# Optimization experiments

Measured on AMD Instinct MI355X. Metric: run time of the kernel, lower is better.

The kernel has to match this reference:

```python
import jax, jax.numpy as jnp
import numpy as np

# Model constants (match init_kwargs)
H, P, N, G, NL, K = 32, 64, 128, 1, 15, 4   # heads, head_dim, state, groups, lambda levels, conv width
HID, T, BATCH = 1024, 1024, 1
INTER = H * P                    # 2048
CONV_DIM = INTER + 2 * G * N     # 2304
PROJ = INTER + CONV_DIM + H * (NL + 1)  # 4864
EPS = 1e-5


def _level_matrix(t_len: int) -> np.ndarray:
    """Fenwick-tree level assignment: for query t, prefix [0,t] splits into
    power-of-two segments from binary expansion of t+1; segment of length 2^l -> level l."""
    lm = np.zeros((t_len, t_len), dtype=np.int32)
    for t in range(t_len):
        n = t + 1
        while n > 0:
            lb = n & (-n)
            lm[t, n - lb:n] = lb.bit_length() - 1
            n -= lb
    return lm


def setup_inputs() -> dict:
    key = jax.random.key(0)
    ks = jax.random.split(key, 4)
    return {
        "hidden_states": jax.random.normal(ks[0], (BATCH, T, HID), jnp.float32),
        "in_proj_w": jax.random.normal(ks[1], (PROJ, HID), jnp.float32) / np.sqrt(HID).astype(np.float32),
        "in_proj_b": jnp.zeros((PROJ,), jnp.float32),
        "conv_w": jax.random.normal(ks[2], (CONV_DIM, K), jnp.float32) / np.sqrt(K).astype(np.float32),
        "dt_bias": jnp.ones((H,), jnp.float32),
        "A_log": jnp.log(jnp.arange(1, H + 1, dtype=jnp.float32)),
        "L_param": jnp.ones((H, NL), jnp.float32),
        "D": jnp.ones((H,), jnp.float32),
        "rmsnorm_w": jnp.ones((INTER,), jnp.float32),
        "out_proj_w": jax.random.normal(ks[3], (HID, INTER), jnp.float32) / np.sqrt(INTER).astype(np.float32),
        "out_proj_b": jnp.zeros((HID,), jnp.float32),
        "level_mat": jnp.asarray(_level_matrix(T)),  # (T,T) int32, data-independent
    }


def reference(hidden_states, in_proj_w, in_proj_b, conv_w, dt_bias, A_log,
              L_param, D, rmsnorm_w, out_proj_w, out_proj_b, level_mat):
    b, t, _ = hidden_states.shape
    # in_proj and split: [z | xBC | dt | dl]
    zxbcdtdl = hidden_states @ in_proj_w.T + in_proj_b
    z, xBC, dt, dl = jnp.split(zxbcdtdl, [INTER, INTER + CONV_DIM, INTER + CONV_DIM + H], axis=-1)
    # depthwise causal conv1d (width K) + SiLU
    xp = jnp.pad(xBC, ((0, 0), (K - 1, 0), (0, 0)))
    conv = sum(xp[:, w:w + t, :] * conv_w[:, w] for w in range(K))
    xBC = jax.nn.silu(conv)
    x, Bm, Cm = jnp.split(xBC, [INTER, INTER + G * N], axis=-1)
    x = x.reshape(b, t, H, P)          # v pre-scale
    Bm = Bm.reshape(b, t, G, N)        # keys
    Cm = Cm.reshape(b, t, G, N)        # queries
    dl = dl.reshape(b, t, H, NL)
    # D residual uses unscaled x (matches hmamba_chunk_scan_combined ordering)
    D_res = x * D[None, None, :, None]
    dt = jax.nn.softplus(dt + dt_bias)            # (b,t,H)
    v = x * dt[..., None]                          # (b,t,H,P)
    A = -jnp.exp(A_log)                            # (H,)
    g = A * dt                                     # (b,t,H), per-token log-decay (<=0)
    Ls = jax.nn.softplus(L_param * dl)             # (b,t,H,NL) per-token level scales
    # cumulative log-decay; decay(t,s) = exp(cg_t - cg_s), s<=t
    cg = jnp.cumsum(g, axis=1).transpose(0, 2, 1)  # (b,H,t)
    mask = jnp.tril(jnp.ones((t, t), bool))
    logdecay = jnp.where(mask, cg[:, :, :, None] - cg[:, :, None, :], -jnp.inf)
    decay = jnp.exp(logdecay)                      # (b,H,t,s)
    # hierarchical level scale H[t,s] = Ls[b,t,h, level(t,s)]
    Hmat = jnp.take_along_axis(Ls.transpose(0, 2, 1, 3), level_mat[None, None, :, :], axis=-1)  # (b,H,t,s)
    scores = jnp.einsum('btgn,bsgn->bgts', Cm, Bm)  # (b,G,t,s), G=1 broadcasts over heads
    att = scores * decay * Hmat                     # (b,H,t,s), masked via decay=0
    y = jnp.einsum('bhts,bshp->bthp', att, v) + D_res
    y = y.reshape(b, t, INTER)
    # gated RMSNorm with norm_before_gate=False: normalize(y * silu(z)) * w
    yg = y * jax.nn.silu(z)
    y = yg * jax.lax.rsqrt(jnp.mean(yg * yg, axis=-1, keepdims=True) + EPS) * rmsnorm_w
    return y @ out_proj_w.T + out_proj_b
```

## Files before the change

kernel.cpp:

```cpp
#include <hip/hip_runtime.h>
#include <hip/hip_bf16.h>
#include <math.h>

#define T_LEN 1024
#define HID 1024
#define NHEAD 32
#define HDIM 64
#define NSTATE 128
#define NLVL 15
#define KCONV 4
#define INTER 2048
#define CONV_DIM 2304
#define PROJ 4864
#define EPS 1e-5f
#define TPROJ ((size_t)T_LEN * PROJ)

typedef __attribute__((ext_vector_type(8))) _Float16 half8;
typedef __attribute__((ext_vector_type(4))) _Float16 half4;
typedef __attribute__((ext_vector_type(4))) float float4v;
typedef unsigned short ushort_t;

__device__ __forceinline__ float softplus_f(float x) {
  return fmaxf(x, 0.f) + log1pf(expf(-fabsf(x)));
}
__device__ __forceinline__ float silu_f(float x) {
  return x / (1.f + expf(-x));
}
__device__ __forceinline__ ushort_t f2h(float f) {
  union { _Float16 h; ushort_t u; } v;
  v.h = (_Float16)f;
  return v.u;
}
__device__ __forceinline__ float h2f(ushort_t u) {
  union { ushort_t u; _Float16 h; } v;
  v.u = u;
  return (float)v.h;
}
__device__ __forceinline__ void gload_lds16(const void* g, void* l) {
  __builtin_amdgcn_global_load_lds(
      (const __attribute__((address_space(1))) void*)g,
      (__attribute__((address_space(3))) void*)l, 16, 0, 0);
}

#define N4_HS  (T_LEN * HID / 4)
#define N4_WI  (PROJ * HID / 4)
#define N4_WO  (HID * INTER / 4)
__global__ __launch_bounds__(256) void prep_f16(
    const float* __restrict__ hs, const float* __restrict__ wi,
    const float* __restrict__ wo, ushort_t* __restrict__ hsb,
    ushort_t* __restrict__ wib, ushort_t* __restrict__ wob) {
  int i = blockIdx.x * 256 + threadIdx.x;
  const float* src; ushort_t* dst; int j;
  if (i < N4_HS)              { src = hs; dst = hsb; j = i; }
  else if (i < N4_HS + N4_WI) { src = wi; dst = wib; j = i - N4_HS; }
  else                        { src = wo; dst = wob; j = i - N4_HS - N4_WI; }
  float4 v = reinterpret_cast<const float4*>(src)[j];
  union { ushort_t u[4]; unsigned long long ll; } o;
  o.u[0] = f2h(v.x); o.u[1] = f2h(v.y); o.u[2] = f2h(v.z); o.u[3] = f2h(v.w);
  reinterpret_cast<unsigned long long*>(dst)[j] = o.ll;
}

__global__ __launch_bounds__(256) void gemm_f16_sk(
    const ushort_t* __restrict__ A, const ushort_t* __restrict__ B,
    ushort_t* __restrict__ Cpart, int M, int N, int K, int Kc) {
  __shared__ ushort_t As[2][128][32];
  __shared__ ushort_t Bs[2][128][32];
  const int tid = threadIdx.x;
  const int w = tid >> 6, L = tid & 63;
  const int n0 = blockIdx.x * 128, m0 = blockIdx.y * 128;
  const int kbeg = blockIdx.z * Kc;
  ushort_t* __restrict__ C = Cpart + (size_t)blockIdx.z * M * N;
  const int mq = (w & 1) * 64, nq = (w >> 1) * 64;
  const int srow = (L >> 2);
  const int sch = (L & 3) * 8;

  float4v acc[4][4];
#pragma unroll
  for (int i = 0; i < 4; ++i)
#pragma unroll
    for (int j = 0; j < 4; ++j) acc[i][j] = (float4v){0.f, 0.f, 0.f, 0.f};

  const int niter = Kc / 32;
  {
    const int kk = kbeg;
#pragma unroll
    for (int j = 0; j < 2; ++j) {
      int r0 = 16 * (w * 2 + j);
      gload_lds16(A + (size_t)(m0 + r0 + srow) * K + kk + sch, &As[0][r0][0]);
      gload_lds16(B + (size_t)(n0 + r0 + srow) * K + kk + sch, &Bs[0][r0][0]);
    }
  }
  for (int it = 0; it < niter; ++it) {
    __syncthreads();
    if (it + 1 < niter) {
      const int kk = kbeg + (it + 1) * 32;
      const int nb = (it + 1) & 1;
#pragma unroll
      for (int j = 0; j < 2; ++j) {
        int r0 = 16 * (w * 2 + j);
        gload_lds16(A + (size_t)(m0 + r0 + srow) * K + kk + sch, &As[nb][r0][0]);
        gload_lds16(B + (size_t)(n0 + r0 + srow) * K + kk + sch, &Bs[nb][r0][0]);
      }
    }
    const int cb = it & 1;
    half8 af[4], bf[4];
#pragma unroll
    for (int t = 0; t < 4; ++t) {
      af[t] = *reinterpret_cast<const half8*>(&As[cb][mq + t * 16 + (L & 15)][(L >> 4) * 8]);
      bf[t] = *reinterpret_cast<const half8*>(&Bs[cb][nq + t * 16 + (L & 15)][(L >> 4) * 8]);
    }
#pragma unroll
    for (int mt = 0; mt < 4; ++mt)
#pragma unroll
      for (int nt = 0; nt < 4; ++nt)
        acc[mt][nt] = __builtin_amdgcn_mfma_f32_16x16x32_f16(af[mt], bf[nt], acc[mt][nt], 0, 0, 0);
  }
  const int qrow = (L >> 4) * 4;
#pragma unroll
  for (int mt = 0; mt < 4; ++mt) {
#pragma unroll
    for (int nt = 0; nt < 4; ++nt) {
      int col = n0 + nq + nt * 16 + (L & 15);
#pragma unroll
      for (int r = 0; r < 4; ++r) {
        int row = m0 + mq + mt * 16 + qrow + r;
        C[(size_t)row * N + col] = f2h(acc[mt][nt][r]);
      }
    }
  }
}

__global__ __launch_bounds__(256) void reduce_out8(const ushort_t* __restrict__ p,
                                                   const float* __restrict__ bias,
                                                   float* __restrict__ out, int MN) {
  int i = blockIdx.x * 256 + threadIdx.x;
  if (i * 8 >= MN) return;
  float o[8] = {0.f, 0.f, 0.f, 0.f, 0.f, 0.f, 0.f, 0.f};
#pragma unroll
  for (int z = 0; z < 8; ++z) {
    half8 v = reinterpret_cast<const half8*>(p + (size_t)z * MN)[i];
#pragma unroll
    for (int j = 0; j < 8; ++j) o[j] += (float)v[j];
  }
  int col = (i * 8) & (HID - 1);
#pragma unroll
  for (int j = 0; j < 8; ++j) o[j] += bias[col + j];
  float4 o0 = {o[0], o[1], o[2], o[3]}, o1 = {o[4], o[5], o[6], o[7]};
  reinterpret_cast<float4*>(out)[i * 2] = o0;
  reinterpret_cast<float4*>(out)[i * 2 + 1] = o1;
}

__global__ __launch_bounds__(64) void scan_g(
    const ushort_t* __restrict__ zh, const float* __restrict__ in_b,
    const float* __restrict__ dt_bias, const float* __restrict__ A_log,
    float* __restrict__ dtb, double* __restrict__ cgd) {
  const int h = blockIdx.x, l = threadIdx.x;
  const int c = INTER + CONV_DIM + h;
  const float bb = in_b[c] + dt_bias[h];
  const float Ae = -expf(A_log[h]);
  double pre[16];
  double acc = 0.0;
#pragma unroll
  for (int i = 0; i < 16; ++i) {
    int t = l * 16 + i;
    size_t o = (size_t)t * PROJ + c;
    float x = h2f(zh[o]) + h2f(zh[TPROJ + o]) + h2f(zh[2 * TPROJ + o]) +
              h2f(zh[3 * TPROJ + o]) + bb;
    float dt = softplus_f(x);
    dtb[t * NHEAD + h] = dt;
    acc += (double)(Ae * dt);
    pre[i] = acc;
  }
  double s = acc;
#pragma unroll
  for (int off = 1; off < 64; off <<= 1) {
    double o = __shfl_up(s, off, 64);
    if (l >= off) s += o;
  }
  const double base = s - acc;
  double* cr = cgd + (size_t)h * T_LEN + l * 16;
#pragma unroll
  for (int i = 0; i < 16; ++i) cr[i] = base + pre[i];
}

__global__ __launch_bounds__(256) void conv_fused(
    const ushort_t* __restrict__ zh, const float* __restrict__ in_b,
    const float* __restrict__ conv_w, const float* __restrict__ dtb,
    const float* __restrict__ Dp, ushort_t* __restrict__ vt,
    float* __restrict__ ybuf, ushort_t* __restrict__ Bb,
    ushort_t* __restrict__ Cb) {
  __shared__ float Xl[67][68];
  __shared__ ushort_t Vl[64][68];
  __shared__ float dtl[64];
  const int tq = blockIdx.x, cy = blockIdx.y;
  const int t0 = tq * 64;
  const int tid = threadIdx.x;
  const int lane = tid & 63, g = tid >> 6;
  const bool vpath = (cy < 32);
  const int c0 = vpath ? cy * 64 : INTER + (cy - 32) * 64;
  if (vpath && tid < 64) dtl[tid] = dtb[(t0 + tid) * NHEAD + cy];

  for (int u = tid; u < 67 * 8; u += 256) {
    int r = u >> 3, c8 = (u & 7) * 8;
    int t = t0 - 3 + r;
    float xs[8];
    if (t >= 0) {
      size_t o = (size_t)t * PROJ + INTER + c0 + c8;
      half8 a = *reinterpret_cast<const half8*>(zh + o);
      half8 b = *reinterpret_cast<const half8*>(zh + TPROJ + o);
      half8 c = *reinterpret_cast<const half8*>(zh + 2 * TPROJ + o);
      half8 d = *reinterpret_cast<const half8*>(zh + 3 * TPROJ + o);
#pragma unroll
      for (int j = 0; j < 8; ++j)
        xs[j] = (float)a[j] + (float)b[j] + (float)c[j] + (float)d[j] +
                in_b[INTER + c0 + c8 + j];
    } else {
#pragma unroll
      for (int j = 0; j < 8; ++j) xs[j] = 0.f;
    }
#pragma unroll
    for (int j = 0; j < 8; ++j) Xl[r][c8 + j] = xs[j];
  }
  __syncthreads();

  const int ccol = c0 + lane;
  const float4 cwv = *reinterpret_cast<const float4*>(conv_w + ccol * KCONV);
  const float Dh = vpath ? Dp[cy] : 0.f;
  float xv[19];
#pragma unroll
  for (int i = 0; i < 19; ++i) xv[i] = Xl[g * 16 + i][lane];
#pragma unroll
  for (int i = 0; i < 16; ++i) {
    float acc = xv[i] * cwv.x + xv[i + 1] * cwv.y + xv[i + 2] * cwv.z + xv[i + 3] * cwv.w;
    float sil = silu_f(acc);
    int tl = g * 16 + i;
    int t = t0 + tl;
    if (vpath) {
      Vl[tl][lane] = f2h(sil * dtl[tl]);
      ybuf[(size_t)t * INTER + c0 + lane] = sil * Dh;
    } else if (ccol < INTER + NSTATE) {
      Bb[t * NSTATE + (ccol - INTER)] = f2h(sil);
    } else {
      Cb[t * NSTATE + (ccol - INTER - NSTATE)] = f2h(sil);
    }
  }
  if (vpath) {
    __syncthreads();
#pragma unroll
    for (int rep = 0; rep < 2; ++rep) {
      int u = tid + 256 * rep;
      int p = u >> 3, t8 = (u & 7) * 8;
      union { ushort_t u16[8]; half8 h; } o;
#pragma unroll
      for (int j = 0; j < 8; ++j) o.u16[j] = Vl[t8 + j][p];
      *reinterpret_cast<half8*>(vt + (size_t)(c0 + p) * T_LEN + t0 + t8) = o.h;
    }
  }
}

__global__ __launch_bounds__(256) void attn_mfma(
    const ushort_t* __restrict__ Bb, const ushort_t* __restrict__ Cb,
    const ushort_t* __restrict__ vt, const double* __restrict__ cgd,
    const ushort_t* __restrict__ zh, const float* __restrict__ in_b,
    const float* __restrict__ L_param, float* __restrict__ ybuf) {
  __shared__ ushort_t Bl[64][136];
  __shared__ ushort_t Vtl[64][72];
  __shared__ float Lsl[64][16];
  __shared__ float cgq[64];
  __shared__ float cgs[64];

  const int item = blockIdx.x;
  const int h = item / 40;
  const int rem = item - h * 40;
  int qt, j;
  if (rem < 4)        { qt = rem;                 j = 0; }
  else if (rem < 12)  { qt = 4 + (rem - 4) / 2;   j = (rem - 4) % 2; }
  else if (rem < 24)  { qt = 8 + (rem - 12) / 3;  j = (rem - 12) % 3; }
  else                { qt = 12 + (rem - 24) / 4; j = (rem - 24) % 4; }

  const int tid = threadIdx.x;
  const int w = tid >> 6, L = tid & 63;
  const int tq0 = qt * 64;
  const double* cgh = cgd + (size_t)h * T_LEN;
  const double base = cgh[tq0];

  for (int i = tid; i < 64 * NLVL; i += 256) {
    int r = i / NLVL, l = i - r * NLVL;
    int cc = INTER + CONV_DIM + NHEAD + h * NLVL + l;
    size_t o = (size_t)(tq0 + r) * PROJ + cc;
    float x = h2f(zh[o]) + h2f(zh[TPROJ + o]) + h2f(zh[2 * TPROJ + o]) +
              h2f(zh[3 * TPROJ + o]) + in_b[cc];
    Lsl[r][l] = softplus_f(L_param[h * NLVL + l] * x);
  }
  if (tid < 64) cgq[tid] = (float)(cgh[tq0 + tid] - base);

  half8 cfrag[4];
  {
    const ushort_t* cr = Cb + (size_t)(tq0 + w * 16 + (L & 15)) * NSTATE + (L >> 4) * 8;
#pragma unroll
    for (int ks = 0; ks < 4; ++ks)
      cfrag[ks] = *reinterpret_cast<const half8*>(cr + ks * 32);
  }
  float4v yac[4];
#pragma unroll
  for (int i = 0; i < 4; ++i) yac[i] = (float4v){0.f, 0.f, 0.f, 0.f};

  __syncthreads();
  const int qS = w * 16 + (L & 15);
  const float cq = cgq[qS];
  const float* Lsq = &Lsl[qS][0];
  const int tgp1 = tq0 + qS + 1;
  const int sbase = (L >> 4) * 4;

  const int st0 = 4 * j;
  const int st1 = min(4 * j + 4, qt + 1);
  for (int st = st0; st < st1; ++st) {
    const int ts0 = st * 64;
    __syncthreads();
#pragma unroll
    for (int i = 0; i < 4; ++i) {
      int u = tid + 256 * i;
      int row = u >> 4, kb = (u & 15) * 8;
      *reinterpret_cast<half8*>(&Bl[row][kb]) =
          *reinterpret_cast<const half8*>(Bb + (size_t)(ts0 + row) * NSTATE + kb);
    }
#pragma unroll
    for (int i = 0; i < 2; ++i) {
      int u = tid + 256 * i;
      int p = u >> 3, sc = (u & 7) * 8;
      *reinterpret_cast<half8*>(&Vtl[p][sc]) =
          *reinterpret_cast<const half8*>(vt + (size_t)(h * HDIM + p) * T_LEN + ts0 + sc);
    }
    if (tid < 64) cgs[tid] = (float)(cgh[ts0 + tid] - base);
    __syncthreads();

    float4v sac[4];
#pragma unroll
    for (int nt = 0; nt < 4; ++nt) sac[nt] = (float4v){0.f, 0.f, 0.f, 0.f};
#pragma unroll
    for (int ks = 0; ks < 4; ++ks) {
#pragma unroll
      for (int nt = 0; nt < 4; ++nt) {
        half8 bfrag = *reinterpret_cast<const half8*>(&Bl[nt * 16 + (L & 15)][ks * 32 + (L >> 4) * 8]);
        sac[nt] = __builtin_amdgcn_mfma_f32_16x16x32_f16(bfrag, cfrag[ks], sac[nt], 0, 0, 0);
      }
    }
#pragma unroll
    for (int nt = 0; nt < 4; ++nt) {
      float4 c4 = *reinterpret_cast<const float4*>(&cgs[nt * 16 + sbase]);
      float cv[4] = {c4.x, c4.y, c4.z, c4.w};
      half4 sv;
#pragma unroll
      for (int r = 0; r < 4; ++r) {
        int sg = ts0 + nt * 16 + sbase + r;
        float val = 0.f;
        if (sg < tgp1) {
          int lvl = 31 - __clz((unsigned)(sg ^ tgp1));
          val = sac[nt][r] * __expf(cq - cv[r]) * Lsq[lvl];
        }
        sv[r] = (_Float16)val;
      }
#pragma unroll
      for (int pt = 0; pt < 4; ++pt) {
        half4 bv = *reinterpret_cast<const half4*>(&Vtl[pt * 16 + (L & 15)][nt * 16 + sbase]);
        yac[pt] = __builtin_amdgcn_mfma_f32_16x16x16f16(sv, bv, yac[pt], 0, 0, 0);
      }
    }
  }
  const int qrow = w * 16 + ((L >> 4) << 2);
#pragma unroll
  for (int pt = 0; pt < 4; ++pt) {
    int p = pt * 16 + (L & 15);
#pragma unroll
    for (int r = 0; r < 4; ++r) {
      int q = qrow + r;
      atomicAdd(ybuf + (size_t)(tq0 + q) * INTER + h * HDIM + p, yac[pt][r]);
    }
  }
}

__global__ __launch_bounds__(256) void rmsnorm_gate(
    const float* __restrict__ ybuf, const ushort_t* __restrict__ zh,
    const float* __restrict__ in_b, const float* __restrict__ w,
    ushort_t* __restrict__ yhf) {
  __shared__ float red[4];
  const int t = blockIdx.x, tid = threadIdx.x;
  const size_t ro = (size_t)t * PROJ + tid * 8;
  const float* yrow = ybuf + (size_t)t * INTER + tid * 8;
  half8 a = *reinterpret_cast<const half8*>(zh + ro);
  half8 b = *reinterpret_cast<const half8*>(zh + TPROJ + ro);
  half8 c = *reinterpret_cast<const half8*>(zh + 2 * TPROJ + ro);
  half8 d = *reinterpret_cast<const half8*>(zh + 3 * TPROJ + ro);
  float4 y0 = reinterpret_cast<const float4*>(yrow)[0];
  float4 y1 = reinterpret_cast<const float4*>(yrow)[1];
  float yv[8] = {y0.x, y0.y, y0.z, y0.w, y1.x, y1.y, y1.z, y1.w};
  float yg[8];
  float ss = 0.f;
#pragma unroll
  for (int j = 0; j < 8; ++j) {
    float z = (float)a[j] + (float)b[j] + (float)c[j] + (float)d[j] + in_b[tid * 8 + j];
    float g = yv[j] * silu_f(z);
    yg[j] = g;
    ss += g * g;
  }
#pragma unroll
  for (int off = 32; off; off >>= 1) ss += __shfl_down(ss, off, 64);
  if ((tid & 63) == 0) red[tid >> 6] = ss;
  __syncthreads();
  if (tid == 0) red[0] = red[0] + red[1] + red[2] + red[3];
  __syncthreads();
  const float scale = rsqrtf(red[0] / (float)INTER + EPS);
  union { ushort_t u[8]; half8 h; } o;
#pragma unroll
  for (int j = 0; j < 8; ++j) o.u[j] = f2h(yg[j] * scale * w[tid * 8 + j]);
  *reinterpret_cast<half8*>(yhf + (size_t)t * INTER + tid * 8) = o.h;
}

extern "C" void kernel_launch(void* const* d_in, const int* in_sizes, int n_in,
                              void* d_out, int out_size, void* d_ws, size_t ws_size,
                              hipStream_t stream) {
  const float* hs        = (const float*)d_in[0];
  const float* in_proj_w = (const float*)d_in[1];
  const float* in_proj_b = (const float*)d_in[2];
  const float* conv_w    = (const float*)d_in[3];
  const float* dt_bias   = (const float*)d_in[4];
  const float* A_log     = (const float*)d_in[5];
  const float* L_param   = (const float*)d_in[6];
  const float* Dp        = (const float*)d_in[7];
  const float* rms_w     = (const float*)d_in[8];
  const float* out_proj_w= (const float*)d_in[9];
  const float* out_proj_b= (const float*)d_in[10];
  float* out = (float*)d_out;

  char* W = (char*)d_ws;
  size_t off = 0;
  auto alloc = [&](size_t bytes) { void* p = W + off; off = (off + bytes + 255) & ~(size_t)255; return p; };
  double*   cgd = (double*)  alloc((size_t)NHEAD * T_LEN * 8);
  ushort_t* zh  = (ushort_t*)alloc((size_t)4 * TPROJ * 2);
  ushort_t* opp = (ushort_t*)alloc((size_t)8 * T_LEN * HID * 2);
  float*    ybuf= (float*)   alloc((size_t)T_LEN * INTER * 4);
  float*    dtb = (float*)   alloc((size_t)T_LEN * NHEAD * 4);
  ushort_t* hsb = (ushort_t*)alloc((size_t)T_LEN * HID * 2);
  ushort_t* Wib = (ushort_t*)alloc((size_t)PROJ * HID * 2);
  ushort_t* Wob = (ushort_t*)alloc((size_t)HID * INTER * 2);
  ushort_t* yhf = (ushort_t*)alloc((size_t)T_LEN * INTER * 2);
  ushort_t* vt  = (ushort_t*)alloc((size_t)T_LEN * INTER * 2);
  ushort_t* Bb  = (ushort_t*)alloc((size_t)T_LEN * NSTATE * 2);
  ushort_t* Cb  = (ushort_t*)alloc((size_t)T_LEN * NSTATE * 2);

  prep_f16<<<(N4_HS + N4_WI + N4_WO) / 256, 256, 0, stream>>>(
      hs, in_proj_w, out_proj_w, hsb, Wib, Wob);

  gemm_f16_sk<<<dim3(PROJ / 128, T_LEN / 128, 4), 256, 0, stream>>>(
      hsb, Wib, zh, T_LEN, PROJ, HID, HID / 4);

  scan_g<<<NHEAD, 64, 0, stream>>>(zh, in_proj_b, dt_bias, A_log, dtb, cgd);

  conv_fused<<<dim3(T_LEN / 64, 36), 256, 0, stream>>>(
      zh, in_proj_b, conv_w, dtb, Dp, vt, ybuf, Bb, Cb);

  attn_mfma<<<NHEAD * 40, 256, 0, stream>>>(Bb, Cb, vt, cgd, zh, in_proj_b,
                                            L_param, ybuf);

  rmsnorm_gate<<<T_LEN, 256, 0, stream>>>(ybuf, zh, in_proj_b, rms_w, yhf);

  gemm_f16_sk<<<dim3(HID / 128, T_LEN / 128, 8), 256, 0, stream>>>(
      yhf, Wob, opp, T_LEN, HID, INTER, INTER / 8);
  reduce_out8<<<(T_LEN * HID / 8 + 255) / 256, 256, 0, stream>>>(
      opp, out_proj_b, out, T_LEN * HID);
}
```

Baseline: 202.8 us.

## Restructure attention kernel to single-wave blocks with register-resident fragments

```diff
diff --git a/kernel.cpp b/kernel.cpp
--- a/kernel.cpp
+++ b/kernel.cpp
@@ -258,123 +258,117 @@
   }
 }
 
-__global__ __launch_bounds__(256) void attn_mfma(
+__global__ __launch_bounds__(64, 2) void attn_mfma(
     const ushort_t* __restrict__ Bb, const ushort_t* __restrict__ Cb,
     const ushort_t* __restrict__ vt, const double* __restrict__ cgd,
     const ushort_t* __restrict__ zh, const float* __restrict__ in_b,
     const float* __restrict__ L_param, float* __restrict__ ybuf) {
-  __shared__ ushort_t Bl[64][136];
-  __shared__ ushort_t Vtl[64][72];
   __shared__ float Lsl[64][16];
-  __shared__ float cgq[64];
-  __shared__ float cgs[64];
 
   const int item = blockIdx.x;
-  const int h = item / 40;
-  const int rem = item - h * 40;
-  int qt, j;
-  if (rem < 4)        { qt = rem;                 j = 0; }
-  else if (rem < 12)  { qt = 4 + (rem - 4) / 2;   j = (rem - 4) % 2; }
-  else if (rem < 24)  { qt = 8 + (rem - 12) / 3;  j = (rem - 12) % 3; }
-  else                { qt = 12 + (rem - 24) / 4; j = (rem - 24) % 4; }
-
-  const int tid = threadIdx.x;
-  const int w = tid >> 6, L = tid & 63;
+  const int h = item / 51;
+  int rem = item - h * 51;
+  int qt = 0;
+#pragma unroll
+  for (int q = 0; q < 16; ++q) {
+    int c = (q + 3) / 3;
+    if (rem < c) { qt = q; break; }
+    rem -= c;
+  }
+  const int jc = rem;
+
+  const int L = threadIdx.x;
   const int tq0 = qt * 64;
   const double* cgh = cgd + (size_t)h * T_LEN;
   const double base = cgh[tq0];
 
-  for (int i = tid; i < 64 * NLVL; i += 256) {
-    int r = i / NLVL, l = i - r * NLVL;
-    int cc = INTER + CONV_DIM + NHEAD + h * NLVL + l;
-    size_t o = (size_t)(tq0 + r) * PROJ + cc;
-    float x = h2f(zh[o]) + h2f(zh[TPROJ + o]) + h2f(zh[2 * TPROJ + o]) +
-              h2f(zh[3 * TPROJ + o]) + in_b[cc];
-    Lsl[r][l] = softplus_f(L_param[h * NLVL + l] * x);
-  }
-  if (tid < 64) cgq[tid] = (float)(cgh[tq0 + tid] - base);
-
-  half8 cfrag[4];
   {
-    const ushort_t* cr = Cb + (size_t)(tq0 + w * 16 + (L & 15)) * NSTATE + (L >> 4) * 8;
+    const int cc0 = INTER + CONV_DIM + NHEAD + h * NLVL;
+    const size_t o = (size_t)(tq0 + L) * PROJ + cc0;
+#pragma unroll
+    for (int l = 0; l < NLVL; ++l) {
+      float x = h2f(zh[o + l]) + h2f(zh[TPROJ + o + l]) +
+                h2f(zh[2 * TPROJ + o + l]) + h2f(zh[3 * TPROJ + o + l]) + in_b[cc0 + l];
+      Lsl[L][l] = softplus_f(L_param[h * NLVL + l] * x);
+    }
+    Lsl[L][NLVL] = 0.f;
+  }
+
+  half8 cfrag[4][4];
+  float cq[4];
+#pragma unroll
+  for (int m = 0; m < 4; ++m) {
+    const ushort_t* cr = Cb + (size_t)(tq0 + m * 16 + (L & 15)) * NSTATE + (L >> 4) * 8;
 #pragma unroll
     for (int ks = 0; ks < 4; ++ks)
-      cfrag[ks] = *reinterpret_cast<const half8*>(cr + ks * 32);
-  }
-  float4v yac[4];
-#pragma unroll
-  for (int i = 0; i < 4; ++i) yac[i] = (float4v){0.f, 0.f, 0.f, 0.f};
-
-  __syncthreads();
-  const int qS = w * 16 + (L & 15);
-  const float cq = cgq[qS];
-  const float* Lsq = &Lsl[qS][0];
-  const int tgp1 = tq0 + qS + 1;
+      cfrag[m][ks] = *reinterpret_cast<const half8*>(cr + ks * 32);
+    cq[m] = (float)(cgh[tq0 + m * 16 + (L & 15)] - base);
+  }
+  float4v yac[4][4];
+#pragma unroll
+  for (int m = 0; m < 4; ++m)
+#pragma unroll
+    for (int pt = 0; pt < 4; ++pt) yac[m][pt] = (float4v){0.f, 0.f, 0.f, 0.f};
+
   const int sbase = (L >> 4) * 4;
-
-  const int st0 = 4 * j;
-  const int st1 = min(4 * j + 4, qt + 1);
+  __builtin_amdgcn_s_waitcnt(0xC07F);
+
+  const int st0 = 3 * jc;
+  const int st1 = min(3 * jc + 3, qt + 1);
   for (int st = st0; st < st1; ++st) {
     const int ts0 = st * 64;
-    __syncthreads();
-#pragma unroll
-    for (int i = 0; i < 4; ++i) {
-      int u = tid + 256 * i;
-      int row = u >> 4, kb = (u & 15) * 8;
-      *reinterpret_cast<half8*>(&Bl[row][kb]) =
-          *reinterpret_cast<const half8*>(Bb + (size_t)(ts0 + row) * NSTATE + kb);
-    }
-#pragma unroll
-    for (int i = 0; i < 2; ++i) {
-      int u = tid + 256 * i;
-      int p = u >> 3, sc = (u & 7) * 8;
-      *reinterpret_cast<half8*>(&Vtl[p][sc]) =
-          *reinterpret_cast<const half8*>(vt + (size_t)(h * HDIM + p) * T_LEN + ts0 + sc);
-    }
-    if (tid < 64) cgs[tid] = (float)(cgh[ts0 + tid] - base);
-    __syncthreads();
-
-    float4v sac[4];
-#pragma unroll
-    for (int nt = 0; nt < 4; ++nt) sac[nt] = (float4v){0.f, 0.f, 0.f, 0.f};
-#pragma unroll
-    for (int ks = 0; ks < 4; ++ks) {
-#pragma unroll
-      for (int nt = 0; nt < 4; ++nt) {
-        half8 bfrag = *reinterpret_cast<const half8*>(&Bl[nt * 16 + (L & 15)][ks * 32 + (L >> 4) * 8]);
-        sac[nt] = __builtin_amdgcn_mfma_f32_16x16x32_f16(bfrag, cfrag[ks], sac[nt], 0, 0, 0);
+#pragma unroll
+    for (int nt = 0; nt < 4; ++nt) {
+      const int s0 = ts0 + nt * 16;
+      half8 bfr[4];
+      const ushort_t* br = Bb + (size_t)(s0 + (L & 15)) * NSTATE + (L >> 4) * 8;
+#pragma unroll
+      for (int ks = 0; ks < 4; ++ks)
+        bfr[ks] = *reinterpret_cast<const half8*>(br + ks * 32);
+      half4 vfr[4];
+#pragma unroll
+      for (int pt = 0; pt < 4; ++pt)
+        vfr[pt] = *reinterpret_cast<const half4*>(
+            vt + (size_t)(h * HDIM + pt * 16 + (L & 15)) * T_LEN + s0 + sbase);
+      double2 cd0 = *reinterpret_cast<const double2*>(cgh + s0 + sbase);
+      double2 cd1 = *reinterpret_cast<const double2*>(cgh + s0 + sbase + 2);
+      float cs[4] = {(float)(cd0.x - base), (float)(cd0.y - base),
+                     (float)(cd1.x - base), (float)(cd1.y - base)};
+#pragma unroll
+      for (int m = 0; m < 4; ++m) {
+        float4v sac = (float4v){0.f, 0.f, 0.f, 0.f};
+#pragma unroll
+        for (int ks = 0; ks < 4; ++ks)
+          sac = __builtin_amdgcn_mfma_f32_16x16x32_f16(bfr[ks], cfrag[m][ks], sac, 0, 0, 0);
+        const int qS = m * 16 + (L & 15);
+        const int tgp1 = tq0 + qS + 1;
+        half4 sv;
+#pragma unroll
+        for (int r = 0; r < 4; ++r) {
+          int sg = s0 + sbase + r;
+          float val = 0.f;
+          if (sg < tgp1) {
+            int lvl = 31 - __clz((unsigned)(sg ^ tgp1));
+            val = sac[r] * __expf(cq[m] - cs[r]) * Lsl[qS][lvl];
+          }
+          sv[r] = (_Float16)val;
+        }
+#pragma unroll
+        for (int pt = 0; pt < 4; ++pt)
+          yac[m][pt] = __builtin_amdgcn_mfma_f32_16x16x16f16(sv, vfr[pt], yac[m][pt], 0, 0, 0);
       }
     }
-#pragma unroll
-    for (int nt = 0; nt < 4; ++nt) {
-      float4 c4 = *reinterpret_cast<const float4*>(&cgs[nt * 16 + sbase]);
-      float cv[4] = {c4.x, c4.y, c4.z, c4.w};
-      half4 sv;
+  }
+#pragma unroll
+  for (int m = 0; m < 4; ++m) {
+#pragma unroll
+    for (int pt = 0; pt < 4; ++pt) {
+      int p = pt * 16 + (L & 15);
 #pragma unroll
       for (int r = 0; r < 4; ++r) {
-        int sg = ts0 + nt * 16 + sbase + r;
-        float val = 0.f;
-        if (sg < tgp1) {
-          int lvl = 31 - __clz((unsigned)(sg ^ tgp1));
-          val = sac[nt][r] * __expf(cq - cv[r]) * Lsq[lvl];
-        }
-        sv[r] = (_Float16)val;
+        int q = m * 16 + sbase + r;
+        atomicAdd(ybuf + (size_t)(tq0 + q) * INTER + h * HDIM + p, yac[m][pt][r]);
       }
-#pragma unroll
-      for (int pt = 0; pt < 4; ++pt) {
-        half4 bv = *reinterpret_cast<const half4*>(&Vtl[pt * 16 + (L & 15)][nt * 16 + sbase]);
-        yac[pt] = __builtin_amdgcn_mfma_f32_16x16x16f16(sv, bv, yac[pt], 0, 0, 0);
-      }
-    }
-  }
-  const int qrow = w * 16 + ((L >> 4) << 2);
-#pragma unroll
-  for (int pt = 0; pt < 4; ++pt) {
-    int p = pt * 16 + (L & 15);
-#pragma unroll
-    for (int r = 0; r < 4; ++r) {
-      int q = qrow + r;
-      atomicAdd(ybuf + (size_t)(tq0 + q) * INTER + h * HDIM + p, yac[pt][r]);
     }
   }
 }
@@ -459,8 +453,8 @@
   conv_fused<<<dim3(T_LEN / 64, 36), 256, 0, stream>>>(
       zh, in_proj_b, conv_w, dtb, Dp, vt, ybuf, Bb, Cb);
 
-  attn_mfma<<<NHEAD * 40, 256, 0, stream>>>(Bb, Cb, vt, cgd, zh, in_proj_b,
-                                            L_param, ybuf);
+  attn_mfma<<<NHEAD * 51, 64, 0, stream>>>(Bb, Cb, vt, cgd, zh, in_proj_b,
+                                           L_param, ybuf);
 
   rmsnorm_gate<<<T_LEN, 256, 0, stream>>>(ybuf, zh, in_proj_b, rms_w, yhf);
 
```

Result: slower. 214.9 us (+6.0%).
